# Kernel tuning notes

Hardware: AMD Instinct MI355X
Metric: run time of the kernel (lower is better)

Reference implementation:

```python
import jax, jax.numpy as jnp
import numpy as np

B, N, C, D = 4, 4096, 1024, 32  # batch, tokens, channels, head dim
EPS = 1e-15
PAD_VAL = 1.0


def setup_inputs() -> dict:
    key = jax.random.key(0)
    k1, k2, k3 = jax.random.split(key, 3)
    x = jax.random.normal(k1, (B, N, C), dtype=jnp.float32)
    W_qkv = jax.random.normal(k2, (3 * C, C), dtype=jnp.float32) * 0.02
    W_proj = jax.random.normal(k3, (C, C), dtype=jnp.float32) * 0.02
    b_proj = jnp.zeros((C,), dtype=jnp.float32)
    return {"x": x, "W_qkv": W_qkv, "W_proj": W_proj, "b_proj": b_proj}


def reference(x, W_qkv, W_proj, b_proj):
    Bx, Nx, Cx = x.shape
    h = Cx // D
    # qkv projection (no bias), then split as torch: reshape(B,N,3,C).permute(0,2,3,1)
    qkv = jnp.einsum('bnc,oc->bno', x, W_qkv)            # [B,N,3C]
    qkv = qkv.reshape(Bx, Nx, 3, Cx).transpose(0, 2, 3, 1)  # [B,3,C,N]
    q, k, v = qkv[:, 0], qkv[:, 1], qkv[:, 2]
    q = jax.nn.relu(q.reshape(Bx, h, D, Nx))             # [B,h,D,N]
    k = jax.nn.relu(k.reshape(Bx, h, D, Nx)).transpose(0, 1, 3, 2)  # [B,h,N,D]
    v = v.reshape(Bx, h, D, Nx)                          # [B,h,D,N]
    # pad v with a row of PAD_VAL=1 to carry the normalizer
    v = jnp.concatenate([v, jnp.full((Bx, h, 1, Nx), PAD_VAL, v.dtype)], axis=2)  # [B,h,D+1,N]
    vk = jnp.einsum('bhdn,bhne->bhde', v, k)             # [B,h,D+1,D]
    out = jnp.einsum('bhde,bhen->bhdn', vk, q)           # [B,h,D+1,N]
    out = out[:, :, :-1] / (out[:, :, -1:] + EPS)        # [B,h,D,N]
    out = out.reshape(Bx, Cx, Nx).transpose(0, 2, 1)     # [B,N,C]
    return jnp.einsum('bnc,oc->bno', out, W_proj) + b_proj
```

## Files before the change

### kernel.cpp

```cpp
#include <hip/hip_runtime.h>


using us8   = __attribute__((ext_vector_type(8))) unsigned short;
using us4   = __attribute__((ext_vector_type(4))) unsigned short;
using s8v   = __attribute__((ext_vector_type(8))) short;
using f32x4 = __attribute__((ext_vector_type(4))) float;

__device__ __forceinline__ unsigned short f2bf(float f) {
    union { float f; unsigned int u; } c; c.f = f;
    unsigned int r = c.u + 0x7fffu + ((c.u >> 16) & 1u);
    return (unsigned short)(r >> 16);
}
__device__ __forceinline__ float bf2f(unsigned short u) {
    union { unsigned int u; float f; } c; c.u = ((unsigned int)u) << 16;
    return c.f;
}

__device__ __forceinline__ void async16(const unsigned short* g, unsigned short* l) {
    __builtin_amdgcn_global_load_lds(
        (const __attribute__((address_space(1))) unsigned int*)g,
        (__attribute__((address_space(3))) unsigned int*)l, 16, 0, 0);
}

__global__ __launch_bounds__(256)
void prep(const float* __restrict__ x, const float* __restrict__ wq,
          const float* __restrict__ wp, unsigned short* __restrict__ xb,
          unsigned short* __restrict__ wqb, unsigned short* __restrict__ wpb) {
    const int NX = 16777216 / 8, NQ = 3145728 / 8, NP = 1048576 / 8;
    int gid = blockIdx.x * 256 + threadIdx.x;
    const float* in; unsigned short* out; int i;
    if (gid < NX)                { in = x;  out = xb;  i = gid * 8; }
    else if (gid < NX + NQ)      { in = wq; out = wqb; i = (gid - NX) * 8; }
    else if (gid < NX + NQ + NP) { in = wp; out = wpb; i = (gid - NX - NQ) * 8; }
    else return;
    float4 a = *(const float4*)(in + i);
    float4 b = *(const float4*)(in + i + 4);
    us8 o;
    o[0] = f2bf(a.x); o[1] = f2bf(a.y); o[2] = f2bf(a.z); o[3] = f2bf(a.w);
    o[4] = f2bf(b.x); o[5] = f2bf(b.y); o[6] = f2bf(b.z); o[7] = f2bf(b.w);
    *(us8*)(out + i) = o;
}

constexpr int TSZ = 16384;

#define FENCE() asm volatile("" ::: "memory")
#define BARX()  do { FENCE(); __builtin_amdgcn_s_barrier(); FENCE(); } while (0)

#define STAGE(KT, BS)                                                        \
  do {                                                                       \
    async16(Ag + g0 + (KT), (BS) + d0);                                      \
    async16(Ag + g1 + (KT), (BS) + d1);                                      \
    async16(Bg + g0 + (KT), (BS) + 8192 + d0);                               \
    async16(Bg + g1 + (KT), (BS) + 8192 + d1);                               \
  } while (0)

template <int MODE>
__device__ __forceinline__
void gemm_core256(const unsigned short* __restrict__ A,
                  const unsigned short* __restrict__ Bt,
                  unsigned short* __restrict__ Cq,
                  unsigned short* __restrict__ kvT,
                  float* __restrict__ Cf, const float* __restrict__ bias,
                  int N, int tM, int tN, unsigned short* lds) {
    const int t    = threadIdx.x;
    const int lane = t & 63;
    const int wv   = t >> 6;
    const int wr   = wv >> 2;
    const int wc   = wv & 3;
    const int mrow = lane & 15;
    const int kq   = lane >> 4;

    const int c0 = t, c1 = 512 + t;
    const int r0 = c0 >> 2, r1 = c1 >> 2;
    const int g0 = r0 * 1024 + ((c0 & 3) ^ ((r0 >> 1) & 3)) * 8;
    const int g1 = r1 * 1024 + ((c1 & 3) ^ ((r1 >> 1) & 3)) * 8;
    const unsigned short* Ag = A  + (size_t)tM * 1024;
    const unsigned short* Bg = Bt + (size_t)tN * 1024;
    const int d0 = wv * 512, d1 = 4096 + wv * 512;

    const int swz  = (kq ^ ((mrow >> 1) & 3)) * 8;
    const int aoff = (wr * 128 + mrow) * 32 + swz;
    const int boff = (wc * 64  + mrow) * 32 + swz;

    f32x4 acc[8][4] = {};
    s8v af[8], bf[4];

    constexpr int NT = 32;

    STAGE(0,  lds);
    STAGE(32, lds + TSZ);
    asm volatile("s_waitcnt vmcnt(4)" ::: "memory");
    BARX();

    unsigned short* bR = lds;
    unsigned short* bT = lds + TSZ;
    unsigned short* bS = lds + 2 * TSZ;

    for (int g = 0; g < NT; ++g) {
        const int kt = (g + 2 < NT ? g + 2 : NT - 1) * 32;
        STAGE(kt, bS);
        FENCE();
#pragma unroll
        for (int mi = 0; mi < 8; ++mi)
            af[mi] = *(const s8v*)&bR[aoff + mi * 512];
#pragma unroll
        for (int ni = 0; ni < 4; ++ni)
            bf[ni] = *(const s8v*)&bR[8192 + boff + ni * 512];
        __builtin_amdgcn_s_setprio(1);
#pragma unroll
        for (int mi = 0; mi < 8; ++mi)
#pragma unroll
            for (int ni = 0; ni < 4; ++ni)
                acc[mi][ni] = __builtin_amdgcn_mfma_f32_16x16x32_bf16(
                    af[mi], bf[ni], acc[mi][ni], 0, 0, 0);
        __builtin_amdgcn_s_setprio(0);
        asm volatile("s_waitcnt vmcnt(4)" ::: "memory");
        BARX();
        unsigned short* tmp = bR; bR = bT; bT = bS; bS = tmp;
    }

    const int crow0 = kq * 4;
    const int ccol  = mrow;
    if (MODE == 0) {
        if (tN >= 1024) {
            const int b2  = tM >> 12;
            const int nb0 = (tM & 4095) + wr * 128;
#pragma unroll
            for (int mi = 0; mi < 8; ++mi) {
                const int nbase = nb0 + mi * 16 + crow0;
#pragma unroll
                for (int ni = 0; ni < 4; ++ni) {
                    const int col = tN + wc * 64 + ni * 16 + ccol;
                    f32x4 v = acc[mi][ni];
                    if (col < 2048) {
                        v[0] = fmaxf(v[0], 0.f); v[1] = fmaxf(v[1], 0.f);
                        v[2] = fmaxf(v[2], 0.f); v[3] = fmaxf(v[3], 0.f);
                    }
                    us4 o;
                    o[0] = f2bf(v[0]); o[1] = f2bf(v[1]);
                    o[2] = f2bf(v[2]); o[3] = f2bf(v[3]);
                    *(us4*)&kvT[((size_t)b2 * 2048 + (col - 1024)) * 4096 + nbase] = o;
                }
            }
        } else {
#pragma unroll
            for (int mi = 0; mi < 8; ++mi)
#pragma unroll
                for (int ni = 0; ni < 4; ++ni) {
                    const int row = tM + wr * 128 + mi * 16 + crow0;
                    const int col = tN + wc * 64 + ni * 16 + ccol;
#pragma unroll
                    for (int r2 = 0; r2 < 4; ++r2)
                        Cq[(size_t)(row + r2) * 1024 + col] =
                            f2bf(fmaxf(acc[mi][ni][r2], 0.f));
                }
        }
    } else {
#pragma unroll
        for (int mi = 0; mi < 8; ++mi)
#pragma unroll
            for (int ni = 0; ni < 4; ++ni) {
                const int row = tM + wr * 128 + mi * 16 + crow0;
                const int col = tN + wc * 64 + ni * 16 + ccol;
#pragma unroll
                for (int r2 = 0; r2 < 4; ++r2)
                    Cf[(size_t)(row + r2) * N + col] = acc[mi][ni][r2] + bias[col];
            }
    }
    asm volatile("s_waitcnt vmcnt(0)" ::: "memory");
}

__device__ __forceinline__ void xcd_map256(int blk, int MT, int& tM, int& tN) {
    const int xcd = blk & 7;
    const int i   = blk >> 3;
    const int MTx = MT >> 3;
    const int ppan = MTx * 4;
    const int p   = i / ppan;
    const int i2  = i % ppan;
    tM = (xcd * MTx + (i2 >> 2)) * 256;
    tN = (p * 4 + (i2 & 3)) * 256;
}

__global__ __launch_bounds__(512, 2)
void gemm_qkv(const unsigned short* __restrict__ A,
              const unsigned short* __restrict__ Bt,
              unsigned short* __restrict__ Cq, unsigned short* __restrict__ kvT,
              int M, int N) {
    extern __shared__ unsigned short lds[];
    int tM, tN;
    xcd_map256(blockIdx.x, M >> 8, tM, tN);
    gemm_core256<0>(A, Bt, Cq, kvT, nullptr, nullptr, N, tM, tN, lds);
}

__global__ __launch_bounds__(512, 2)
void gemm_proj(const unsigned short* __restrict__ A,
               const unsigned short* __restrict__ Bt,
               float* __restrict__ C, const float* __restrict__ bias,
               int M, int N) {
    extern __shared__ unsigned short lds[];
    int tM, tN;
    xcd_map256(blockIdx.x, M >> 8, tM, tN);
    gemm_core256<1>(A, Bt, nullptr, nullptr, C, bias, N, tM, tN, lds);
}

__global__ __launch_bounds__(256)
void lite_vk(const unsigned short* __restrict__ kvT, float* __restrict__ vkws) {
    const int bh = blockIdx.x, ck = blockIdx.y;
    const int b = bh >> 5, h = bh & 31;
    const int S = 136;
    __shared__ unsigned short Ks[32 * S];
    __shared__ unsigned short Vs[32 * S];
    __shared__ float Rs[4][1088];
    const int t = threadIdx.x, lane = t & 63, wv = t >> 6;
    const unsigned short* Kp = kvT + ((size_t)b * 2048 + h * 32) * 4096 + ck * 512;
    const unsigned short* Vp = kvT + ((size_t)b * 2048 + 1024 + h * 32) * 4096 + ck * 512;
    const int sr = t >> 3, ss = (t & 7) * 16;
    f32x4 acc00 = {}, acc01 = {}, acc10 = {}, acc11 = {}, accO0 = {}, accO1 = {};
    s8v ones;
#pragma unroll
    for (int j = 0; j < 8; ++j) ones[j] = (short)0x3F80;
    const int mrow = lane & 15, kq = (lane >> 4) * 8;

    for (int tile = 0; tile < 4; ++tile) {
        int go = tile * 128 + ss;
        us8 k0v = *(const us8*)(Kp + (size_t)sr * 4096 + go);
        us8 k1v = *(const us8*)(Kp + (size_t)sr * 4096 + go + 8);
        us8 v0v = *(const us8*)(Vp + (size_t)sr * 4096 + go);
        us8 v1v = *(const us8*)(Vp + (size_t)sr * 4096 + go + 8);
        __syncthreads();
        *(us8*)&Ks[sr * S + ss]     = k0v;
        *(us8*)&Ks[sr * S + ss + 8] = k1v;
        *(us8*)&Vs[sr * S + ss]     = v0v;
        *(us8*)&Vs[sr * S + ss + 8] = v1v;
        __syncthreads();
        int ko = wv * 32 + kq;
        s8v a0 = *(const s8v*)&Vs[(mrow)      * S + ko];
        s8v a1 = *(const s8v*)&Vs[(16 + mrow) * S + ko];
        s8v b0 = *(const s8v*)&Ks[(mrow)      * S + ko];
        s8v b1 = *(const s8v*)&Ks[(16 + mrow) * S + ko];
        acc00 = __builtin_amdgcn_mfma_f32_16x16x32_bf16(a0, b0, acc00, 0, 0, 0);
        acc01 = __builtin_amdgcn_mfma_f32_16x16x32_bf16(a0, b1, acc01, 0, 0, 0);
        acc10 = __builtin_amdgcn_mfma_f32_16x16x32_bf16(a1, b0, acc10, 0, 0, 0);
        acc11 = __builtin_amdgcn_mfma_f32_16x16x32_bf16(a1, b1, acc11, 0, 0, 0);
        accO0 = __builtin_amdgcn_mfma_f32_16x16x32_bf16(ones, b0, accO0, 0, 0, 0);
        accO1 = __builtin_amdgcn_mfma_f32_16x16x32_bf16(ones, b1, accO1, 0, 0, 0);
    }

    const int ccol = lane & 15, crow = (lane >> 4) * 4;
    float* R = Rs[wv];
#pragma unroll
    for (int r2 = 0; r2 < 4; ++r2) {
        R[(crow + r2) * 32 + ccol]           = acc00[r2];
        R[(crow + r2) * 32 + 16 + ccol]      = acc01[r2];
        R[(16 + crow + r2) * 32 + ccol]      = acc10[r2];
        R[(16 + crow + r2) * 32 + 16 + ccol] = acc11[r2];
    }
    if ((lane >> 4) == 0) {
        R[1024 + ccol]      = accO0[0];
        R[1024 + 16 + ccol] = accO1[0];
    }
    __syncthreads();
    float* vkb = vkws + ((size_t)ck * 128 + bh) * 1056;
    for (int i = t; i < 1056; i += 256) {
        vkb[i] = Rs[0][i] + Rs[1][i] + Rs[2][i] + Rs[3][i];
    }
}

__global__ __launch_bounds__(256)
void lite_apply(const unsigned short* __restrict__ qb,
                const float* __restrict__ vkws,
                unsigned short* __restrict__ yb) {
    const int bh = blockIdx.x, nb = blockIdx.y;
    const int b = bh >> 5, h = bh & 31;
    __shared__ unsigned short vkh[48 * 32];
    __shared__ unsigned short vkl[48 * 32];
    const int t = threadIdx.x;
    for (int i = t; i < 48 * 32; i += 256) {
        float v = 0.f;
        if (i < 33 * 32) {
#pragma unroll
            for (int p = 0; p < 8; ++p)
                v += vkws[((size_t)p * 128 + bh) * 1056 + i];
        }
        unsigned short hi = f2bf(v);
        vkh[i] = hi;
        vkl[i] = f2bf(v - bf2f(hi));
    }
    __syncthreads();

    const int lane = t & 63, wv = t >> 6;
    const int col = lane & 15, quad = lane >> 4;
    s8v b0h = *(const s8v*)&vkh[(col)      * 32 + quad * 8];
    s8v b0l = *(const s8v*)&vkl[(col)      * 32 + quad * 8];
    s8v b1h = *(const s8v*)&vkh[(16 + col) * 32 + quad * 8];
    s8v b1l = *(const s8v*)&vkl[(16 + col) * 32 + quad * 8];
    s8v b2h = *(const s8v*)&vkh[(32 + col) * 32 + quad * 8];
    s8v b2l = *(const s8v*)&vkl[(32 + col) * 32 + quad * 8];

    const int ntile = nb * 256 + wv * 64;
#pragma unroll
    for (int mi = 0; mi < 4; ++mi) {
        int tok = ntile + mi * 16 + col;
        const unsigned short* qp =
            qb + (size_t)(b * 4096 + tok) * 1024 + h * 32 + quad * 8;
        s8v a = *(const s8v*)qp;
        f32x4 n0 = {}, n1 = {}, dd = {};
        n0 = __builtin_amdgcn_mfma_f32_16x16x32_bf16(b0h, a, n0, 0, 0, 0);
        n0 = __builtin_amdgcn_mfma_f32_16x16x32_bf16(b0l, a, n0, 0, 0, 0);
        n1 = __builtin_amdgcn_mfma_f32_16x16x32_bf16(b1h, a, n1, 0, 0, 0);
        n1 = __builtin_amdgcn_mfma_f32_16x16x32_bf16(b1l, a, n1, 0, 0, 0);
        dd = __builtin_amdgcn_mfma_f32_16x16x32_bf16(b2h, a, dd, 0, 0, 0);
        dd = __builtin_amdgcn_mfma_f32_16x16x32_bf16(b2l, a, dd, 0, 0, 0);
        float den  = __shfl(dd[0], col, 64);
        float rinv = 1.f / (den + 1e-15f);
        us4 o0, o1;
#pragma unroll
        for (int r = 0; r < 4; ++r) {
            o0[r] = f2bf(n0[r] * rinv);
            o1[r] = f2bf(n1[r] * rinv);
        }
        size_t o = (size_t)(b * 4096 + tok) * 1024 + h * 32;
        *(us4*)&yb[o + quad * 4]      = o0;
        *(us4*)&yb[o + 16 + quad * 4] = o1;
    }
}

extern "C" void kernel_launch(void* const* d_in, const int* in_sizes, int n_in,
                              void* d_out, int out_size, void* d_ws, size_t ws_size,
                              hipStream_t stream) {
    const float* x     = (const float*)d_in[0];
    const float* Wqkv  = (const float*)d_in[1];
    const float* Wproj = (const float*)d_in[2];
    const float* bproj = (const float*)d_in[3];
    float* out = (float*)d_out;

    const int M = 16384, Cdim = 1024, O1 = 3072;

    unsigned short* xb     = (unsigned short*)d_ws;
    unsigned short* wqkvb  = xb + (size_t)M * Cdim;
    unsigned short* wprojb = wqkvb + (size_t)O1 * Cdim;
    unsigned short* qb     = wprojb + (size_t)Cdim * Cdim;
    unsigned short* kvT    = qb + (size_t)M * Cdim;
    unsigned short* ybuf   = kvT + (size_t)4 * 2048 * 4096;
    float* vkws            = (float*)(ybuf + (size_t)M * Cdim);

    static int attr_done = 0;
    if (!attr_done) {
        hipFuncSetAttribute((const void*)gemm_qkv,
                            hipFuncAttributeMaxDynamicSharedMemorySize, 98304);
        hipFuncSetAttribute((const void*)gemm_proj,
                            hipFuncAttributeMaxDynamicSharedMemorySize, 98304);
        attr_done = 1;
    }

    const int PREP_GROUPS = (16777216 + 3145728 + 1048576) / 8;
    prep<<<(PREP_GROUPS + 255) / 256, 256, 0, stream>>>(
        x, Wqkv, Wproj, xb, wqkvb, wprojb);

    gemm_qkv<<<(M / 256) * (O1 / 256), 512, 98304, stream>>>(
        xb, wqkvb, qb, kvT, M, O1);

    lite_vk<<<dim3(128, 8), 256, 0, stream>>>(kvT, vkws);
    lite_apply<<<dim3(128, 16), 256, 0, stream>>>(qb, vkws, ybuf);

    gemm_proj<<<(M / 256) * (Cdim / 256), 512, 98304, stream>>>(
        ybuf, wprojb, out, bproj, M, Cdim);
}
```

Baseline: 317.5 us.

## Fuse V·Kᵀ reduction into QKV GEMM epilogue and drop the lite_vk kernel

The prep kernel now permutes W_qkv rows so that each 64-column slice of the K/V output holds 32 K columns and their matching 32 V columns for one head. In the QKV GEMM epilogue, each wave stages its ReLU'd K tile and V tile through LDS and computes partial V·Kᵀ and the ones·K normalizer with MFMA, writing fp32 partials per 128-row slab. The bf16 kvT intermediate and the separate lite_vk kernel go away, and lite_apply now sums 32 partials instead of 8. The async stage issue is also moved after the LDS fragment reads. The trade is a longer GEMM epilogue and an extra barrier for less global traffic and one fewer launch.

Measured after the change: 301.1 us. 5.2% less time.

```diff
diff --git a/kernel.cpp b/kernel.cpp
--- a/kernel.cpp
+++ b/kernel.cpp
@@ -28,17 +28,24 @@
           unsigned short* __restrict__ wqb, unsigned short* __restrict__ wpb) {
     const int NX = 16777216 / 8, NQ = 3145728 / 8, NP = 1048576 / 8;
     int gid = blockIdx.x * 256 + threadIdx.x;
-    const float* in; unsigned short* out; int i;
-    if (gid < NX)                { in = x;  out = xb;  i = gid * 8; }
-    else if (gid < NX + NQ)      { in = wq; out = wqb; i = (gid - NX) * 8; }
-    else if (gid < NX + NQ + NP) { in = wp; out = wpb; i = (gid - NX - NQ) * 8; }
+    const float* in; unsigned short* out; int i, oi;
+    if (gid < NX)                { in = x;  out = xb;  i = gid * 8; oi = i; }
+    else if (gid < NX + NQ) {
+        i = (gid - NX) * 8;
+        int r = i >> 10, cc = i & 1023, rp;
+        if (r < 1024)      rp = r;
+        else if (r < 2048) rp = 1024 + ((r - 1024) >> 5) * 64 + (r & 31);
+        else               rp = 1056 + ((r - 2048) >> 5) * 64 + (r & 31);
+        in = wq; out = wqb; oi = rp * 1024 + cc;
+    }
+    else if (gid < NX + NQ + NP) { in = wp; out = wpb; i = (gid - NX - NQ) * 8; oi = i; }
     else return;
     float4 a = *(const float4*)(in + i);
     float4 b = *(const float4*)(in + i + 4);
     us8 o;
     o[0] = f2bf(a.x); o[1] = f2bf(a.y); o[2] = f2bf(a.z); o[3] = f2bf(a.w);
     o[4] = f2bf(b.x); o[5] = f2bf(b.y); o[6] = f2bf(b.z); o[7] = f2bf(b.w);
-    *(us8*)(out + i) = o;
+    *(us8*)(out + oi) = o;
 }
 
 constexpr int TSZ = 16384;
@@ -59,7 +66,7 @@
 void gemm_core256(const unsigned short* __restrict__ A,
                   const unsigned short* __restrict__ Bt,
                   unsigned short* __restrict__ Cq,
-                  unsigned short* __restrict__ kvT,
+                  float* __restrict__ vkp,
                   float* __restrict__ Cf, const float* __restrict__ bias,
                   int N, int tM, int tN, unsigned short* lds) {
     const int t    = threadIdx.x;
@@ -98,14 +105,13 @@
 
     for (int g = 0; g < NT; ++g) {
         const int kt = (g + 2 < NT ? g + 2 : NT - 1) * 32;
-        STAGE(kt, bS);
-        FENCE();
 #pragma unroll
         for (int mi = 0; mi < 8; ++mi)
             af[mi] = *(const s8v*)&bR[aoff + mi * 512];
 #pragma unroll
         for (int ni = 0; ni < 4; ++ni)
             bf[ni] = *(const s8v*)&bR[8192 + boff + ni * 512];
+        STAGE(kt, bS);
         __builtin_amdgcn_s_setprio(1);
 #pragma unroll
         for (int mi = 0; mi < 8; ++mi)
@@ -119,28 +125,90 @@
         unsigned short* tmp = bR; bR = bT; bT = bS; bS = tmp;
     }
 
+    asm volatile("s_waitcnt vmcnt(0)" ::: "memory");
+    BARX();
+
     const int crow0 = kq * 4;
     const int ccol  = mrow;
     if (MODE == 0) {
         if (tN >= 1024) {
-            const int b2  = tM >> 12;
-            const int nb0 = (tM & 4095) + wr * 128;
+            unsigned short* usW = lds + wv * 6144;
 #pragma unroll
             for (int mi = 0; mi < 8; ++mi) {
-                const int nbase = nb0 + mi * 16 + crow0;
-#pragma unroll
-                for (int ni = 0; ni < 4; ++ni) {
-                    const int col = tN + wc * 64 + ni * 16 + ccol;
-                    f32x4 v = acc[mi][ni];
-                    if (col < 2048) {
-                        v[0] = fmaxf(v[0], 0.f); v[1] = fmaxf(v[1], 0.f);
-                        v[2] = fmaxf(v[2], 0.f); v[3] = fmaxf(v[3], 0.f);
-                    }
+                const int n0 = mi * 16 + kq * 4;
+                const int sub = n0 & 7;
+#pragma unroll
+                for (int ni = 0; ni < 2; ++ni) {
+                    const int e = ni * 16 + mrow;
                     us4 o;
-                    o[0] = f2bf(v[0]); o[1] = f2bf(v[1]);
-                    o[2] = f2bf(v[2]); o[3] = f2bf(v[3]);
-                    *(us4*)&kvT[((size_t)b2 * 2048 + (col - 1024)) * 4096 + nbase] = o;
-                }
+#pragma unroll
+                    for (int r2 = 0; r2 < 4; ++r2)
+                        o[r2] = f2bf(fmaxf(acc[mi][ni][r2], 0.f));
+                    *(us4*)&usW[e * 128 + (((n0 >> 3) ^ e) & 15) * 8 + sub] = o;
+                }
+                us4 ov;
+#pragma unroll
+                for (int r2 = 0; r2 < 4; ++r2)
+                    ov[r2] = f2bf(acc[mi][2][r2]);
+                *(us4*)&usW[4096 + mrow * 128 + (((n0 >> 3) ^ mrow) & 15) * 8 + sub] = ov;
+            }
+            FENCE();
+            s8v bK[2][4], aV[4], ones;
+#pragma unroll
+            for (int j = 0; j < 8; ++j) ones[j] = (short)0x3F80;
+#pragma unroll
+            for (int eblk = 0; eblk < 2; ++eblk)
+#pragma unroll
+                for (int ks = 0; ks < 4; ++ks) {
+                    const int e = eblk * 16 + mrow;
+                    bK[eblk][ks] = *(const s8v*)&usW[e * 128 + (((ks * 4 + kq) ^ mrow) & 15) * 8];
+                }
+#pragma unroll
+            for (int ks = 0; ks < 4; ++ks)
+                aV[ks] = *(const s8v*)&usW[4096 + mrow * 128 + (((ks * 4 + kq) ^ mrow) & 15) * 8];
+            f32x4 vk0[2] = {}, vk1[2] = {}, pd[2] = {};
+#pragma unroll
+            for (int eblk = 0; eblk < 2; ++eblk)
+#pragma unroll
+                for (int ks = 0; ks < 4; ++ks) {
+                    vk0[eblk] = __builtin_amdgcn_mfma_f32_16x16x32_bf16(
+                        aV[ks], bK[eblk][ks], vk0[eblk], 0, 0, 0);
+                    pd[eblk] = __builtin_amdgcn_mfma_f32_16x16x32_bf16(
+                        ones, bK[eblk][ks], pd[eblk], 0, 0, 0);
+                }
+            FENCE();
+#pragma unroll
+            for (int mi = 0; mi < 8; ++mi) {
+                const int n0 = mi * 16 + kq * 4;
+                us4 ov;
+#pragma unroll
+                for (int r2 = 0; r2 < 4; ++r2)
+                    ov[r2] = f2bf(acc[mi][3][r2]);
+                *(us4*)&usW[4096 + mrow * 128 + (((n0 >> 3) ^ mrow) & 15) * 8 + (n0 & 7)] = ov;
+            }
+            FENCE();
+#pragma unroll
+            for (int ks = 0; ks < 4; ++ks)
+                aV[ks] = *(const s8v*)&usW[4096 + mrow * 128 + (((ks * 4 + kq) ^ mrow) & 15) * 8];
+#pragma unroll
+            for (int eblk = 0; eblk < 2; ++eblk)
+#pragma unroll
+                for (int ks = 0; ks < 4; ++ks)
+                    vk1[eblk] = __builtin_amdgcn_mfma_f32_16x16x32_bf16(
+                        aV[ks], bK[eblk][ks], vk1[eblk], 0, 0, 0);
+            const int hh = ((tN - 1024) >> 6) + wc;
+            const int bh = (tM >> 12) * 32 + hh;
+            const int p  = ((tM & 4095) >> 8) * 2 + wr;
+            float* vb = vkp + ((size_t)p * 128 + bh) * 1056;
+#pragma unroll
+            for (int eblk = 0; eblk < 2; ++eblk) {
+                const int e = eblk * 16 + mrow;
+#pragma unroll
+                for (int r = 0; r < 4; ++r) {
+                    vb[(crow0 + r) * 32 + e]      = vk0[eblk][r];
+                    vb[(16 + crow0 + r) * 32 + e] = vk1[eblk][r];
+                }
+                if (kq == 0) vb[1024 + e] = pd[eblk][0];
             }
         } else {
 #pragma unroll
@@ -167,7 +235,6 @@
                     Cf[(size_t)(row + r2) * N + col] = acc[mi][ni][r2] + bias[col];
             }
     }
-    asm volatile("s_waitcnt vmcnt(0)" ::: "memory");
 }
 
 __device__ __forceinline__ void xcd_map256(int blk, int MT, int& tM, int& tN) {
@@ -184,12 +251,12 @@
 __global__ __launch_bounds__(512, 2)
 void gemm_qkv(const unsigned short* __restrict__ A,
               const unsigned short* __restrict__ Bt,
-              unsigned short* __restrict__ Cq, unsigned short* __restrict__ kvT,
+              unsigned short* __restrict__ Cq, float* __restrict__ vkp,
               int M, int N) {
     extern __shared__ unsigned short lds[];
     int tM, tN;
     xcd_map256(blockIdx.x, M >> 8, tM, tN);
-    gemm_core256<0>(A, Bt, Cq, kvT, nullptr, nullptr, N, tM, tN, lds);
+    gemm_core256<0>(A, Bt, Cq, vkp, nullptr, nullptr, N, tM, tN, lds);
 }
 
 __global__ __launch_bounds__(512, 2)
@@ -204,71 +271,8 @@
 }
 
 __global__ __launch_bounds__(256)
-void lite_vk(const unsigned short* __restrict__ kvT, float* __restrict__ vkws) {
-    const int bh = blockIdx.x, ck = blockIdx.y;
-    const int b = bh >> 5, h = bh & 31;
-    const int S = 136;
-    __shared__ unsigned short Ks[32 * S];
-    __shared__ unsigned short Vs[32 * S];
-    __shared__ float Rs[4][1088];
-    const int t = threadIdx.x, lane = t & 63, wv = t >> 6;
-    const unsigned short* Kp = kvT + ((size_t)b * 2048 + h * 32) * 4096 + ck * 512;
-    const unsigned short* Vp = kvT + ((size_t)b * 2048 + 1024 + h * 32) * 4096 + ck * 512;
-    const int sr = t >> 3, ss = (t & 7) * 16;
-    f32x4 acc00 = {}, acc01 = {}, acc10 = {}, acc11 = {}, accO0 = {}, accO1 = {};
-    s8v ones;
-#pragma unroll
-    for (int j = 0; j < 8; ++j) ones[j] = (short)0x3F80;
-    const int mrow = lane & 15, kq = (lane >> 4) * 8;
-
-    for (int tile = 0; tile < 4; ++tile) {
-        int go = tile * 128 + ss;
-        us8 k0v = *(const us8*)(Kp + (size_t)sr * 4096 + go);
-        us8 k1v = *(const us8*)(Kp + (size_t)sr * 4096 + go + 8);
-        us8 v0v = *(const us8*)(Vp + (size_t)sr * 4096 + go);
-        us8 v1v = *(const us8*)(Vp + (size_t)sr * 4096 + go + 8);
-        __syncthreads();
-        *(us8*)&Ks[sr * S + ss]     = k0v;
-        *(us8*)&Ks[sr * S + ss + 8] = k1v;
-        *(us8*)&Vs[sr * S + ss]     = v0v;
-        *(us8*)&Vs[sr * S + ss + 8] = v1v;
-        __syncthreads();
-        int ko = wv * 32 + kq;
-        s8v a0 = *(const s8v*)&Vs[(mrow)      * S + ko];
-        s8v a1 = *(const s8v*)&Vs[(16 + mrow) * S + ko];
-        s8v b0 = *(const s8v*)&Ks[(mrow)      * S + ko];
-        s8v b1 = *(const s8v*)&Ks[(16 + mrow) * S + ko];
-        acc00 = __builtin_amdgcn_mfma_f32_16x16x32_bf16(a0, b0, acc00, 0, 0, 0);
-        acc01 = __builtin_amdgcn_mfma_f32_16x16x32_bf16(a0, b1, acc01, 0, 0, 0);
-        acc10 = __builtin_amdgcn_mfma_f32_16x16x32_bf16(a1, b0, acc10, 0, 0, 0);
-        acc11 = __builtin_amdgcn_mfma_f32_16x16x32_bf16(a1, b1, acc11, 0, 0, 0);
-        accO0 = __builtin_amdgcn_mfma_f32_16x16x32_bf16(ones, b0, accO0, 0, 0, 0);
-        accO1 = __builtin_amdgcn_mfma_f32_16x16x32_bf16(ones, b1, accO1, 0, 0, 0);
-    }
-
-    const int ccol = lane & 15, crow = (lane >> 4) * 4;
-    float* R = Rs[wv];
-#pragma unroll
-    for (int r2 = 0; r2 < 4; ++r2) {
-        R[(crow + r2) * 32 + ccol]           = acc00[r2];
-        R[(crow + r2) * 32 + 16 + ccol]      = acc01[r2];
-        R[(16 + crow + r2) * 32 + ccol]      = acc10[r2];
-        R[(16 + crow + r2) * 32 + 16 + ccol] = acc11[r2];
-    }
-    if ((lane >> 4) == 0) {
-        R[1024 + ccol]      = accO0[0];
-        R[1024 + 16 + ccol] = accO1[0];
-    }
-    __syncthreads();
-    float* vkb = vkws + ((size_t)ck * 128 + bh) * 1056;
-    for (int i = t; i < 1056; i += 256) {
-        vkb[i] = Rs[0][i] + Rs[1][i] + Rs[2][i] + Rs[3][i];
-    }
-}
-
-__global__ __launch_bounds__(256)
 void lite_apply(const unsigned short* __restrict__ qb,
-                const float* __restrict__ vkws,
+                const float* __restrict__ vkp,
                 unsigned short* __restrict__ yb) {
     const int bh = blockIdx.x, nb = blockIdx.y;
     const int b = bh >> 5, h = bh & 31;
@@ -279,8 +283,8 @@
         float v = 0.f;
         if (i < 33 * 32) {
 #pragma unroll
-            for (int p = 0; p < 8; ++p)
-                v += vkws[((size_t)p * 128 + bh) * 1056 + i];
+            for (int p = 0; p < 32; ++p)
+                v += vkp[((size_t)p * 128 + bh) * 1056 + i];
         }
         unsigned short hi = f2bf(v);
         vkh[i] = hi;
@@ -340,9 +344,8 @@
     unsigned short* wqkvb  = xb + (size_t)M * Cdim;
     unsigned short* wprojb = wqkvb + (size_t)O1 * Cdim;
     unsigned short* qb     = wprojb + (size_t)Cdim * Cdim;
-    unsigned short* kvT    = qb + (size_t)M * Cdim;
-    unsigned short* ybuf   = kvT + (size_t)4 * 2048 * 4096;
-    float* vkws            = (float*)(ybuf + (size_t)M * Cdim);
+    unsigned short* ybuf   = qb + (size_t)M * Cdim;
+    float* vkp             = (float*)(ybuf + (size_t)M * Cdim);
 
     static int attr_done = 0;
     if (!attr_done) {
@@ -358,10 +361,9 @@
         x, Wqkv, Wproj, xb, wqkvb, wprojb);
 
     gemm_qkv<<<(M / 256) * (O1 / 256), 512, 98304, stream>>>(
-        xb, wqkvb, qb, kvT, M, O1);
-
-    lite_vk<<<dim3(128, 8), 256, 0, stream>>>(kvT, vkws);
-    lite_apply<<<dim3(128, 16), 256, 0, stream>>>(qb, vkws, ybuf);
+        xb, wqkvb, qb, vkp, M, O1);
+
+    lite_apply<<<dim3(128, 16), 256, 0, stream>>>(qb, vkp, ybuf);
 
     gemm_proj<<<(M / 256) * (Cdim / 256), 512, 98304, stream>>>(
         ybuf, wprojb, out, bproj, M, Cdim);
```
